# Kernel optimization log

Measured on AMD Instinct MI355X. Metric: run time of the kernel, lower is better.

The kernel has to match this reference:

```python
import jax, jax.numpy as jnp
import numpy as np

D_MODEL = 768
N_HEADS = 12
D_K = D_MODEL // N_HEADS
B, S = 4, 2048


def setup_inputs() -> dict:
    key = jax.random.key(0)
    ks = jax.random.split(key, 5)
    x = jax.random.normal(ks[0], (B, S, D_MODEL), dtype=jnp.float32)
    # causal mask, broadcast over batch and heads; 0 -> masked
    mask = jnp.tril(jnp.ones((S, S), dtype=jnp.int32))[None, None, :, :]
    Wqkv = jax.random.normal(ks[1], (D_MODEL, 3 * D_MODEL), dtype=jnp.float32) * (D_MODEL ** -0.5)
    bqkv = jax.random.normal(ks[2], (3 * D_MODEL,), dtype=jnp.float32) * 0.02
    Wout = jax.random.normal(ks[3], (D_MODEL, D_MODEL), dtype=jnp.float32) * (D_MODEL ** -0.5)
    bout = jax.random.normal(ks[4], (D_MODEL,), dtype=jnp.float32) * 0.02
    return {"x": x, "mask": mask, "Wqkv": Wqkv, "bqkv": bqkv, "Wout": Wout, "bout": bout}


def reference(x, mask, Wqkv, bqkv, Wout, bout):
    b, s, d = x.shape
    qkv = x @ Wqkv + bqkv                                   # [b, s, 3d]
    qkv = qkv.reshape(b, s, 3, N_HEADS, D_K)
    qkv = jnp.transpose(qkv, (2, 0, 3, 1, 4))               # [3, b, h, s, d_k]
    q, k, v = qkv[0], qkv[1], qkv[2]
    scores = jnp.einsum("bhqd,bhkd->bhqk", q, k) / (D_K ** 0.5)
    scores = jnp.where(mask == 0, -jnp.inf, scores)
    attn = jax.nn.softmax(scores, axis=-1)                   # dropout = identity (eval)
    out = jnp.einsum("bhqk,bhkd->bhqd", attn, v)             # [b, h, s, d_k]
    out = jnp.transpose(out, (0, 2, 1, 3)).reshape(b, s, d)
    return out @ Wout + bout
```

## Files before the change

### kernel.cpp

```cpp
#include <hip/hip_runtime.h>

typedef __bf16 bf16x8 __attribute__((ext_vector_type(8)));
typedef __bf16 bf16x4 __attribute__((ext_vector_type(4)));
typedef float f32x4 __attribute__((ext_vector_type(4)));

#define D_MODEL 768
#define NH 12
#define DKH 64
#define BATCH 4
#define SEQ 2048
#define ROWS (BATCH*SEQ)
#define N_QKV (3*D_MODEL)
#define QSCALE 0.18033688f

__device__ __forceinline__ float fast_exp2(float x) {
  float r;
  asm("v_exp_f32 %0, %1" : "=v"(r) : "v"(x));
  return r;
}

__global__ void k_convert(const float* __restrict__ in, __bf16* __restrict__ out, int n) {
  int i = (blockIdx.x * blockDim.x + threadIdx.x) * 4;
  if (i >= n) return;
  float4 v = *(const float4*)(in + i);
  bf16x4 o4 = {(__bf16)v.x, (__bf16)v.y, (__bf16)v.z, (__bf16)v.w};
  *(bf16x4*)(out + i) = o4;
}

__global__ void k_transpose(const float* __restrict__ in, __bf16* __restrict__ out, int R, int C) {
  __shared__ float tile[32][33];
  int c0 = blockIdx.x * 32, r0 = blockIdx.y * 32;
  int tx = threadIdx.x, ty = threadIdx.y;
  #pragma unroll
  for (int i = 0; i < 4; ++i) {
    int r = ty + i*8;
    tile[r][tx] = in[(size_t)(r0 + r)*C + c0 + tx];
  }
  __syncthreads();
  #pragma unroll
  for (int i = 0; i < 4; ++i) {
    int c = ty + i*8;
    out[(size_t)(c0 + c)*R + r0 + tx] = (__bf16)tile[tx][c];
  }
}

__device__ __forceinline__ void gemm_stage(const __bf16* __restrict__ A, int lda,
                                           const __bf16* __restrict__ Bt, int ldb,
                                           int m0, int n0, int kt,
                                           __bf16* lA, __bf16* lB) {
  const int tid  = threadIdx.x;
  const int lane = tid & 63;
  const int wid  = tid >> 6;
  #pragma unroll
  for (int c = 0; c < 2; ++c) {
    int chunk = wid*2 + c;
    int bo = chunk*1024 + lane*16;
    int m  = bo >> 6;
    int kb = ((bo & 63) ^ (((m >> 1) & 3) << 4)) >> 1;
    __builtin_amdgcn_global_load_lds(
      (const __attribute__((address_space(1))) void*)(A + (size_t)(m0 + m)*lda + kt + kb),
      (__attribute__((address_space(3))) void*)(lA + chunk*512), 16, 0, 0);
    __builtin_amdgcn_global_load_lds(
      (const __attribute__((address_space(1))) void*)(Bt + (size_t)(n0 + m)*ldb + kt + kb),
      (__attribute__((address_space(3))) void*)(lB + chunk*512), 16, 0, 0);
  }
}

__device__ __forceinline__ void gemm_iter(const __bf16* __restrict__ A, int lda,
                                          const __bf16* __restrict__ Bt, int ldb,
                                          int m0, int n0, int t, int NT,
                                          __bf16* lA, __bf16* lB, int BUF, int NBUF,
                                          int wm, int wn, int lr, int lk,
                                          f32x4 acc[4][4]) {
  if (t + 1 < NT) asm volatile("s_waitcnt vmcnt(4)" ::: "memory");
  else            asm volatile("s_waitcnt vmcnt(0)" ::: "memory");
  __builtin_amdgcn_s_barrier();
  asm volatile("" ::: "memory");
  if (t + 2 < NT)
    gemm_stage(A, lda, Bt, ldb, m0, n0, (t+2)*32, lA + NBUF*4096, lB + NBUF*4096);
  const char* cA = (const char*)(lA + BUF*4096);
  const char* cB = (const char*)(lB + BUF*4096);
  bf16x8 af[4], bfr[4];
  #pragma unroll
  for (int i = 0; i < 4; ++i) {
    int ra = wm + i*16 + lr;
    int rb = wn + i*16 + lr;
    af[i]  = *(const bf16x8*)(cA + ra*64 + ((lk*16) ^ (((ra >> 1) & 3) << 4)));
    bfr[i] = *(const bf16x8*)(cB + rb*64 + ((lk*16) ^ (((rb >> 1) & 3) << 4)));
  }
  #pragma unroll
  for (int mi = 0; mi < 4; ++mi)
    #pragma unroll
    for (int ni = 0; ni < 4; ++ni)
      acc[mi][ni] = __builtin_amdgcn_mfma_f32_16x16x32_bf16(af[mi], bfr[ni], acc[mi][ni], 0, 0, 0);
}

__device__ __forceinline__ void gemm_core(const __bf16* __restrict__ A, int lda,
                                          const __bf16* __restrict__ Bt, int ldb,
                                          int K, int m0, int n0,
                                          __bf16* lA, __bf16* lB, f32x4 acc[4][4]) {
  const int lane = threadIdx.x & 63;
  const int wid  = threadIdx.x >> 6;
  const int wm   = (wid >> 1) * 64;
  const int wn   = (wid & 1) * 64;
  const int lr   = lane & 15;
  const int lk   = lane >> 4;
  const int NT   = K >> 5;

  gemm_stage(A, lda, Bt, ldb, m0, n0, 0,  lA,        lB);
  gemm_stage(A, lda, Bt, ldb, m0, n0, 32, lA + 4096, lB + 4096);

  for (int t = 0; t < NT; t += 3) {
    gemm_iter(A, lda, Bt, ldb, m0, n0, t,   NT, lA, lB, 0, 2, wm, wn, lr, lk, acc);
    gemm_iter(A, lda, Bt, ldb, m0, n0, t+1, NT, lA, lB, 1, 0, wm, wn, lr, lk, acc);
    gemm_iter(A, lda, Bt, ldb, m0, n0, t+2, NT, lA, lB, 2, 1, wm, wn, lr, lk, acc);
  }
}

__global__ __launch_bounds__(256) void k_gemm_qkv(const __bf16* __restrict__ xb,
                                                  const __bf16* __restrict__ wT,
                                                  const float* __restrict__ bias,
                                                  __bf16* __restrict__ qb,
                                                  __bf16* __restrict__ kb,
                                                  __bf16* __restrict__ vtb) {
  __shared__ __align__(16) __bf16 lA[3*128*32];
  __shared__ __align__(16) __bf16 lB[3*128*32];
  f32x4 acc[4][4];
  #pragma unroll
  for (int i = 0; i < 4; ++i)
    #pragma unroll
    for (int j = 0; j < 4; ++j) { f32x4 z = {0.f,0.f,0.f,0.f}; acc[i][j] = z; }

  const int GX = N_QKV/128;
  int bid = blockIdx.y * GX + blockIdx.x;
  int cpx = (GX * ROWS/128) >> 3;
  int swz = (bid & 7) * cpx + (bid >> 3);
  const int m0 = (swz / GX) * 128, n0 = (swz % GX) * 128;
  gemm_core(xb, D_MODEL, wT, D_MODEL, D_MODEL, m0, n0, lA, lB, acc);

  const int lane = threadIdx.x & 63;
  const int wid  = threadIdx.x >> 6;
  const int wm = (wid >> 1) * 64, wn = (wid & 1) * 64;
  const int lr = lane & 15, lk = lane >> 4;
  const int tt = n0 / D_MODEL;

  if (tt < 2) {
    #pragma unroll
    for (int mi = 0; mi < 4; ++mi) {
      #pragma unroll
      for (int ni = 0; ni < 4; ++ni) {
        int col = n0 + wn + ni*16 + lr;
        int r2  = col - tt*D_MODEL;
        int hh  = r2 >> 6, dk = r2 & 63;
        float bv = bias[col];
        #pragma unroll
        for (int j = 0; j < 4; ++j) {
          int row = m0 + wm + mi*16 + lk*4 + j;
          int bb = row >> 11, ss = row & 2047;
          float fv = acc[mi][ni][j] + bv;
          if (tt == 0) qb[(((size_t)bb*NH + hh)*SEQ + ss)*DKH + dk] = (__bf16)(fv * QSCALE);
          else         kb[(((size_t)bb*NH + hh)*SEQ + ss)*DKH + dk] = (__bf16)fv;
        }
      }
    }
  } else {
    __syncthreads();
    __bf16* patch = (wid < 2 ? lA : lB) + (wid & 1)*4096;
    #pragma unroll
    for (int ni = 0; ni < 4; ++ni) {
      int cl = ni*16 + lr;
      float bv = bias[n0 + wn + cl];
      int sw2 = (cl & 7) << 4;
      #pragma unroll
      for (int mi = 0; mi < 4; ++mi) {
        bf16x4 v4;
        #pragma unroll
        for (int j = 0; j < 4; ++j) v4[j] = (__bf16)(acc[mi][ni][j] + bv);
        *(bf16x4*)((char*)patch + ((cl*128 + (mi*16 + lk*4)*2) ^ sw2)) = v4;
      }
    }
    int hh   = (n0 + wn - 2*D_MODEL) >> 6;
    int bb   = m0 >> 11;
    int ssG  = (m0 & 2047) + wm;
    int dk_h = lane >> 4;
    int pb   = (lane & 15) * 4;
    int g    = pb >> 5;
    int tq   = (pb >> 2) & 7;
    int rwb  = g*32 + 16*(tq & 1) + 4*(tq >> 1);
    __bf16* vout = vtb + (((size_t)bb*NH + hh)*DKH)*SEQ + ssG + pb;
    #pragma unroll
    for (int r = 0; r < 16; ++r) {
      int dk = r*4 + dk_h;
      bf16x4 v4 = *(const bf16x4*)((const char*)patch + ((dk*128 + rwb*2) ^ ((dk & 7) << 4)));
      *(bf16x4*)(vout + (size_t)dk*SEQ) = v4;
    }
  }
}

__global__ __launch_bounds__(256) void k_gemm_out(const __bf16* __restrict__ ab,
                                                  const __bf16* __restrict__ wT,
                                                  const float* __restrict__ bias,
                                                  float* __restrict__ out) {
  __shared__ __align__(16) __bf16 lA[3*128*32];
  __shared__ __align__(16) __bf16 lB[3*128*32];
  f32x4 acc[4][4];
  #pragma unroll
  for (int i = 0; i < 4; ++i)
    #pragma unroll
    for (int j = 0; j < 4; ++j) { f32x4 z = {0.f,0.f,0.f,0.f}; acc[i][j] = z; }

  const int GX = D_MODEL/128;
  int bid = blockIdx.y * GX + blockIdx.x;
  int cpx = (GX * ROWS/128) >> 3;
  int swz = (bid & 7) * cpx + (bid >> 3);
  const int m0 = (swz / GX) * 128, n0 = (swz % GX) * 128;
  gemm_core(ab, D_MODEL, wT, D_MODEL, D_MODEL, m0, n0, lA, lB, acc);

  const int lane = threadIdx.x & 63;
  const int wid  = threadIdx.x >> 6;
  const int wm = (wid >> 1) * 64, wn = (wid & 1) * 64;
  const int lr = lane & 15, lk = lane >> 4;
  #pragma unroll
  for (int mi = 0; mi < 4; ++mi) {
    #pragma unroll
    for (int ni = 0; ni < 4; ++ni) {
      int col = n0 + wn + ni*16 + lr;
      float bv = bias[col];
      #pragma unroll
      for (int j = 0; j < 4; ++j) {
        int row = m0 + wm + mi*16 + lk*4 + j;
        out[(size_t)row*D_MODEL + col] = acc[mi][ni][j] + bv;
      }
    }
  }
}

__global__ __launch_bounds__(256) void k_attn(const __bf16* __restrict__ q,
                                              const __bf16* __restrict__ k,
                                              const __bf16* __restrict__ vt,
                                              __bf16* __restrict__ out) {
  __shared__ __align__(16) char lsK[2][8192];
  __shared__ __align__(16) char lsV[2][8192];

  const int tid  = threadIdx.x;
  const int lane = tid & 63;
  const int wid  = tid >> 6;
  const int lr   = lane & 15;
  const int lk   = lane >> 4;

  const int bid  = blockIdx.x;
  const int qi64 = 31 - bid / (BATCH*NH);
  const int bh   = bid % (BATCH*NH);
  const int b    = bh / NH, h = bh - b*NH;
  const int q0w  = qi64*64 + wid*16;
  const int nt   = qi64 + 1;

  const __bf16* qh = q + (size_t)bh*SEQ*DKH;
  const char*   kB = (const char*)(k  + (size_t)bh*SEQ*DKH);
  const char*   vB = (const char*)(vt + (size_t)bh*DKH*SEQ);

  bf16x8 bq[2];
  #pragma unroll
  for (int c = 0; c < 2; ++c)
    bq[c] = *(const bf16x8*)(qh + (size_t)(q0w + lr)*DKH + c*32 + lk*8);

  bf16x8 ones;
  #pragma unroll
  for (int i = 0; i < 8; ++i) ones[i] = (__bf16)1.0f;
  const f32x4 Z4 = {0.f, 0.f, 0.f, 0.f};

  const int offB = lr*128 + ((lk*16) ^ ((lr & 7) << 4));

  f32x4 o[4];
  #pragma unroll
  for (int df = 0; df < 4; ++df) { f32x4 z = {0.f,0.f,0.f,0.f}; o[df] = z; }
  f32x4 o_l = {0.f, 0.f, 0.f, 0.f};

  auto stage = [&](int buf, int kv0) {
    #pragma unroll
    for (int c = 0; c < 2; ++c) {
      int lb   = (wid*2 + c)*1024 + lane*16;
      int row  = lb >> 7;
      int colb = (lb & 127) ^ ((row & 7) << 4);
      __builtin_amdgcn_global_load_lds(
        (const __attribute__((address_space(1))) void*)(kB + (size_t)(kv0 + row)*128 + colb),
        (__attribute__((address_space(3))) void*)(lsK[buf] + (wid*2 + c)*1024), 16, 0, 0);
      __builtin_amdgcn_global_load_lds(
        (const __attribute__((address_space(1))) void*)(vB + (size_t)row*(SEQ*2) + (size_t)kv0*2 + colb),
        (__attribute__((address_space(3))) void*)(lsV[buf] + (wid*2 + c)*1024), 16, 0, 0);
    }
  };

  stage(0, 0);
  __syncthreads();
  int cur = 0;

  for (int t = 0; t < nt; ++t) {
    const int kv0 = t * 64;
    if (t + 1 < nt) stage(cur ^ 1, kv0 + 64);

    {
      const char* kp0 = lsK[cur] + offB;
      const char* kp1 = lsK[cur] + (offB ^ 64);
      const char* vp0 = lsV[cur] + offB;
      const char* vp1 = lsV[cur] + (offB ^ 64);

      f32x4 sc[4];
      __builtin_amdgcn_s_setprio(1);
      #pragma unroll
      for (int n = 0; n < 4; ++n) {
        bf16x8 ak0 = *(const bf16x8*)(kp0 + n*2048);
        bf16x8 ak1 = *(const bf16x8*)(kp1 + n*2048);
        sc[n] = __builtin_amdgcn_mfma_f32_16x16x32_bf16(ak0, bq[0], Z4, 0, 0, 0);
        sc[n] = __builtin_amdgcn_mfma_f32_16x16x32_bf16(ak1, bq[1], sc[n], 0, 0, 0);
      }
      __builtin_amdgcn_s_setprio(0);
      if (kv0 + 63 > q0w) {
        int qrow = q0w + lr;
        #pragma unroll
        for (int n = 0; n < 4; ++n) {
          int kvb = kv0 + n*16 + lk*4;
          #pragma unroll
          for (int j = 0; j < 4; ++j)
            if (kvb + j > qrow) sc[n][j] = -1e30f;
        }
      }
      bf16x8 pa[2];
      #pragma unroll
      for (int n = 0; n < 4; ++n)
        #pragma unroll
        for (int j = 0; j < 4; ++j)
          pa[n >> 1][((n & 1) << 2) | j] = (__bf16)fast_exp2(sc[n][j]);
      __builtin_amdgcn_s_setprio(1);
      o_l = __builtin_amdgcn_mfma_f32_16x16x32_bf16(pa[0], ones, o_l, 0, 0, 0);
      o_l = __builtin_amdgcn_mfma_f32_16x16x32_bf16(pa[1], ones, o_l, 0, 0, 0);
      #pragma unroll
      for (int df = 0; df < 4; ++df) {
        bf16x8 bv0 = *(const bf16x8*)(vp0 + df*2048);
        bf16x8 bv1 = *(const bf16x8*)(vp1 + df*2048);
        o[df] = __builtin_amdgcn_mfma_f32_16x16x32_bf16(pa[0], bv0, o[df], 0, 0, 0);
        o[df] = __builtin_amdgcn_mfma_f32_16x16x32_bf16(pa[1], bv1, o[df], 0, 0, 0);
      }
      __builtin_amdgcn_s_setprio(0);
    }
    __syncthreads();
    cur ^= 1;
  }

  float invl[4];
  #pragma unroll
  for (int j = 0; j < 4; ++j) invl[j] = 1.0f / o_l[j];
  #pragma unroll
  for (int df = 0; df < 4; ++df) {
    int d = df*16 + lr;
    #pragma unroll
    for (int j = 0; j < 4; ++j) {
      int ss = q0w + lk*4 + j;
      out[((size_t)b*SEQ + ss)*D_MODEL + h*DKH + d] = (__bf16)(o[df][j] * invl[j]);
    }
  }
}

extern "C" void kernel_launch(void* const* d_in, const int* in_sizes, int n_in,
                              void* d_out, int out_size, void* d_ws, size_t ws_size,
                              hipStream_t stream) {
  const float* x    = (const float*)d_in[0];
  const float* Wqkv = (const float*)d_in[2];
  const float* bqkv = (const float*)d_in[3];
  const float* Wout = (const float*)d_in[4];
  const float* bout = (const float*)d_in[5];
  float* out = (float*)d_out;

  char* w = (char*)d_ws;
  __bf16* xb    = (__bf16*)w; w += (size_t)ROWS*D_MODEL*2;
  __bf16* wqkvT = (__bf16*)w; w += (size_t)N_QKV*D_MODEL*2;
  __bf16* woutT = (__bf16*)w; w += (size_t)D_MODEL*D_MODEL*2;
  __bf16* qb    = (__bf16*)w; w += (size_t)BATCH*NH*SEQ*DKH*2;
  __bf16* kb    = (__bf16*)w; w += (size_t)BATCH*NH*SEQ*DKH*2;
  __bf16* vtb   = (__bf16*)w; w += (size_t)BATCH*NH*SEQ*DKH*2;
  __bf16* attnb = (__bf16*)w; w += (size_t)ROWS*D_MODEL*2;

  k_convert<<<(ROWS*D_MODEL/4 + 255)/256, 256, 0, stream>>>(x, xb, ROWS*D_MODEL);
  k_transpose<<<dim3(N_QKV/32, D_MODEL/32), dim3(32, 8), 0, stream>>>(Wqkv, wqkvT, D_MODEL, N_QKV);
  k_transpose<<<dim3(D_MODEL/32, D_MODEL/32), dim3(32, 8), 0, stream>>>(Wout, woutT, D_MODEL, D_MODEL);
  k_gemm_qkv<<<dim3(N_QKV/128, ROWS/128), 256, 0, stream>>>(xb, wqkvT, bqkv, qb, kb, vtb);
  k_attn<<<32*BATCH*NH, 256, 0, stream>>>(qb, kb, vtb, attnb);
  k_gemm_out<<<dim3(D_MODEL/128, ROWS/128), 256, 0, stream>>>(attnb, woutT, bout, out);
}
```

Before: 127.8 us.

## Widen QKV GEMM tile to 128x256 with dedicated staging and epilogue

Adds a second GEMM core that computes 128x256 output tiles in the QKV projection, with each wave owning a 64x128 sub-tile and 32 accumulator fragments. This halves the grid size and the number of times A tiles are reloaded, which raises arithmetic intensity per LDS byte. The V-transpose epilogue now handles two heads per wave in sequence. The cost is more accumulator registers (128 VGPRs), which may lower occupancy, plus larger LDS use and fewer blocks (576) to spread across the CUs.

Measured after the change: 144.8 us. +13.3%, slower.

```diff
diff --git a/kernel.cpp b/kernel.cpp
--- a/kernel.cpp
+++ b/kernel.cpp
@@ -117,6 +117,89 @@
   }
 }
 
+__device__ __forceinline__ void gemm_stage2(const __bf16* __restrict__ A, int lda,
+                                            const __bf16* __restrict__ Bt, int ldb,
+                                            int m0, int n0, int kt,
+                                            __bf16* lA, __bf16* lB) {
+  const int tid  = threadIdx.x;
+  const int lane = tid & 63;
+  const int wid  = tid >> 6;
+  #pragma unroll
+  for (int c = 0; c < 2; ++c) {
+    int chunk = wid*2 + c;
+    int bo = chunk*1024 + lane*16;
+    int m  = bo >> 6;
+    int kb = ((bo & 63) ^ (((m >> 1) & 3) << 4)) >> 1;
+    __builtin_amdgcn_global_load_lds(
+      (const __attribute__((address_space(1))) void*)(A + (size_t)(m0 + m)*lda + kt + kb),
+      (__attribute__((address_space(3))) void*)(lA + chunk*512), 16, 0, 0);
+  }
+  #pragma unroll
+  for (int c = 0; c < 4; ++c) {
+    int chunk = wid*4 + c;
+    int bo = chunk*1024 + lane*16;
+    int m  = bo >> 6;
+    int kb = ((bo & 63) ^ (((m >> 1) & 3) << 4)) >> 1;
+    __builtin_amdgcn_global_load_lds(
+      (const __attribute__((address_space(1))) void*)(Bt + (size_t)(n0 + m)*ldb + kt + kb),
+      (__attribute__((address_space(3))) void*)(lB + chunk*512), 16, 0, 0);
+  }
+}
+
+__device__ __forceinline__ void gemm_iter2(const __bf16* __restrict__ A, int lda,
+                                           const __bf16* __restrict__ Bt, int ldb,
+                                           int m0, int n0, int t, int NT,
+                                           __bf16* lA, __bf16* lB, int BUF, int NBUF,
+                                           int wm, int wn, int lr, int lk,
+                                           f32x4 acc[4][8]) {
+  if (t + 1 < NT) asm volatile("s_waitcnt vmcnt(6)" ::: "memory");
+  else            asm volatile("s_waitcnt vmcnt(0)" ::: "memory");
+  __builtin_amdgcn_s_barrier();
+  asm volatile("" ::: "memory");
+  if (t + 2 < NT)
+    gemm_stage2(A, lda, Bt, ldb, m0, n0, (t+2)*32, lA + NBUF*4096, lB + NBUF*8192);
+  const char* cA = (const char*)(lA + BUF*4096);
+  const char* cB = (const char*)(lB + BUF*8192);
+  bf16x8 af[4], bfr[8];
+  #pragma unroll
+  for (int i = 0; i < 4; ++i) {
+    int ra = wm + i*16 + lr;
+    af[i]  = *(const bf16x8*)(cA + ra*64 + ((lk*16) ^ (((ra >> 1) & 3) << 4)));
+  }
+  #pragma unroll
+  for (int i = 0; i < 8; ++i) {
+    int rb = wn + i*16 + lr;
+    bfr[i] = *(const bf16x8*)(cB + rb*64 + ((lk*16) ^ (((rb >> 1) & 3) << 4)));
+  }
+  #pragma unroll
+  for (int mi = 0; mi < 4; ++mi)
+    #pragma unroll
+    for (int ni = 0; ni < 8; ++ni)
+      acc[mi][ni] = __builtin_amdgcn_mfma_f32_16x16x32_bf16(af[mi], bfr[ni], acc[mi][ni], 0, 0, 0);
+}
+
+__device__ __forceinline__ void gemm_core2(const __bf16* __restrict__ A, int lda,
+                                           const __bf16* __restrict__ Bt, int ldb,
+                                           int K, int m0, int n0,
+                                           __bf16* lA, __bf16* lB, f32x4 acc[4][8]) {
+  const int lane = threadIdx.x & 63;
+  const int wid  = threadIdx.x >> 6;
+  const int wm   = (wid >> 1) * 64;
+  const int wn   = (wid & 1) * 128;
+  const int lr   = lane & 15;
+  const int lk   = lane >> 4;
+  const int NT   = K >> 5;
+
+  gemm_stage2(A, lda, Bt, ldb, m0, n0, 0,  lA,        lB);
+  gemm_stage2(A, lda, Bt, ldb, m0, n0, 32, lA + 4096, lB + 8192);
+
+  for (int t = 0; t < NT; t += 3) {
+    gemm_iter2(A, lda, Bt, ldb, m0, n0, t,   NT, lA, lB, 0, 2, wm, wn, lr, lk, acc);
+    gemm_iter2(A, lda, Bt, ldb, m0, n0, t+1, NT, lA, lB, 1, 0, wm, wn, lr, lk, acc);
+    gemm_iter2(A, lda, Bt, ldb, m0, n0, t+2, NT, lA, lB, 2, 1, wm, wn, lr, lk, acc);
+  }
+}
+
 __global__ __launch_bounds__(256) void k_gemm_qkv(const __bf16* __restrict__ xb,
                                                   const __bf16* __restrict__ wT,
                                                   const float* __restrict__ bias,
@@ -124,23 +207,23 @@
                                                   __bf16* __restrict__ kb,
                                                   __bf16* __restrict__ vtb) {
   __shared__ __align__(16) __bf16 lA[3*128*32];
-  __shared__ __align__(16) __bf16 lB[3*128*32];
-  f32x4 acc[4][4];
+  __shared__ __align__(16) __bf16 lB[3*256*32];
+  f32x4 acc[4][8];
   #pragma unroll
   for (int i = 0; i < 4; ++i)
     #pragma unroll
-    for (int j = 0; j < 4; ++j) { f32x4 z = {0.f,0.f,0.f,0.f}; acc[i][j] = z; }
-
-  const int GX = N_QKV/128;
+    for (int j = 0; j < 8; ++j) { f32x4 z = {0.f,0.f,0.f,0.f}; acc[i][j] = z; }
+
+  const int GX = N_QKV/256;
   int bid = blockIdx.y * GX + blockIdx.x;
   int cpx = (GX * ROWS/128) >> 3;
   int swz = (bid & 7) * cpx + (bid >> 3);
-  const int m0 = (swz / GX) * 128, n0 = (swz % GX) * 128;
-  gemm_core(xb, D_MODEL, wT, D_MODEL, D_MODEL, m0, n0, lA, lB, acc);
+  const int m0 = (swz / GX) * 128, n0 = (swz % GX) * 256;
+  gemm_core2(xb, D_MODEL, wT, D_MODEL, D_MODEL, m0, n0, lA, lB, acc);
 
   const int lane = threadIdx.x & 63;
   const int wid  = threadIdx.x >> 6;
-  const int wm = (wid >> 1) * 64, wn = (wid & 1) * 64;
+  const int wm = (wid >> 1) * 64, wn = (wid & 1) * 128;
   const int lr = lane & 15, lk = lane >> 4;
   const int tt = n0 / D_MODEL;
 
@@ -148,7 +231,7 @@
     #pragma unroll
     for (int mi = 0; mi < 4; ++mi) {
       #pragma unroll
-      for (int ni = 0; ni < 4; ++ni) {
+      for (int ni = 0; ni < 8; ++ni) {
         int col = n0 + wn + ni*16 + lr;
         int r2  = col - tt*D_MODEL;
         int hh  = r2 >> 6, dk = r2 & 63;
@@ -165,34 +248,37 @@
     }
   } else {
     __syncthreads();
-    __bf16* patch = (wid < 2 ? lA : lB) + (wid & 1)*4096;
-    #pragma unroll
-    for (int ni = 0; ni < 4; ++ni) {
-      int cl = ni*16 + lr;
-      float bv = bias[n0 + wn + cl];
-      int sw2 = (cl & 7) << 4;
-      #pragma unroll
-      for (int mi = 0; mi < 4; ++mi) {
-        bf16x4 v4;
-        #pragma unroll
-        for (int j = 0; j < 4; ++j) v4[j] = (__bf16)(acc[mi][ni][j] + bv);
-        *(bf16x4*)((char*)patch + ((cl*128 + (mi*16 + lk*4)*2) ^ sw2)) = v4;
-      }
-    }
-    int hh   = (n0 + wn - 2*D_MODEL) >> 6;
-    int bb   = m0 >> 11;
-    int ssG  = (m0 & 2047) + wm;
+    __bf16* patch = lB + wid*4096;
+    int bb  = m0 >> 11;
+    int ssG = (m0 & 2047) + wm;
     int dk_h = lane >> 4;
     int pb   = (lane & 15) * 4;
     int g    = pb >> 5;
     int tq   = (pb >> 2) & 7;
     int rwb  = g*32 + 16*(tq & 1) + 4*(tq >> 1);
-    __bf16* vout = vtb + (((size_t)bb*NH + hh)*DKH)*SEQ + ssG + pb;
-    #pragma unroll
-    for (int r = 0; r < 16; ++r) {
-      int dk = r*4 + dk_h;
-      bf16x4 v4 = *(const bf16x4*)((const char*)patch + ((dk*128 + rwb*2) ^ ((dk & 7) << 4)));
-      *(bf16x4*)(vout + (size_t)dk*SEQ) = v4;
+    #pragma unroll
+    for (int hh2 = 0; hh2 < 2; ++hh2) {
+      #pragma unroll
+      for (int ni2 = 0; ni2 < 4; ++ni2) {
+        int cl = ni2*16 + lr;
+        float bv = bias[n0 + wn + hh2*64 + cl];
+        int sw2 = (cl & 7) << 4;
+        #pragma unroll
+        for (int mi = 0; mi < 4; ++mi) {
+          bf16x4 v4;
+          #pragma unroll
+          for (int j = 0; j < 4; ++j) v4[j] = (__bf16)(acc[mi][hh2*4 + ni2][j] + bv);
+          *(bf16x4*)((char*)patch + ((cl*128 + (mi*16 + lk*4)*2) ^ sw2)) = v4;
+        }
+      }
+      int hh = (n0 + wn + hh2*64 - 2*D_MODEL) >> 6;
+      __bf16* vout = vtb + (((size_t)bb*NH + hh)*DKH)*SEQ + ssG + pb;
+      #pragma unroll
+      for (int r = 0; r < 16; ++r) {
+        int dk = r*4 + dk_h;
+        bf16x4 v4 = *(const bf16x4*)((const char*)patch + ((dk*128 + rwb*2) ^ ((dk & 7) << 4)));
+        *(bf16x4*)(vout + (size_t)dk*SEQ) = v4;
+      }
     }
   }
 }
@@ -383,7 +469,7 @@
   k_convert<<<(ROWS*D_MODEL/4 + 255)/256, 256, 0, stream>>>(x, xb, ROWS*D_MODEL);
   k_transpose<<<dim3(N_QKV/32, D_MODEL/32), dim3(32, 8), 0, stream>>>(Wqkv, wqkvT, D_MODEL, N_QKV);
   k_transpose<<<dim3(D_MODEL/32, D_MODEL/32), dim3(32, 8), 0, stream>>>(Wout, woutT, D_MODEL, D_MODEL);
-  k_gemm_qkv<<<dim3(N_QKV/128, ROWS/128), 256, 0, stream>>>(xb, wqkvT, bqkv, qb, kb, vtb);
+  k_gemm_qkv<<<dim3(N_QKV/256, ROWS/128), 256, 0, stream>>>(xb, wqkvT, bqkv, qb, kb, vtb);
   k_attn<<<32*BATCH*NH, 256, 0, stream>>>(qb, kb, vtb, attnb);
   k_gemm_out<<<dim3(D_MODEL/128, ROWS/128), 256, 0, stream>>>(attnb, woutT, bout, out);
 }
```
